# Kernel tuning notes

Hardware: AMD Instinct MI355X
Metric: run time of the kernel (lower is better)

Reference implementation:

```python
import jax, jax.numpy as jnp
import numpy as np

HIDDEN = 512
INPUT = 512
BATCH = 16384


def _quant_dequant(w):
    # mirrors torch: scale = max(|w|)/127 + 1e-8; int8 round-clamp; dequantize
    scale = jnp.max(jnp.abs(w)) / 127.0 + 1e-8
    q = jnp.clip(jnp.round(w / scale), -128, 127)
    return q * scale


def setup_inputs() -> dict:
    key = jax.random.key(0)
    ks = jax.random.split(key, 7)
    x = jax.random.normal(ks[0], (BATCH, INPUT), dtype=jnp.float32)
    h_prev = jax.random.normal(ks[1], (BATCH, HIDDEN), dtype=jnp.float32)
    c_prev = jax.random.normal(ks[2], (BATCH, HIDDEN), dtype=jnp.float32)
    w_ih = _quant_dequant(jax.random.normal(ks[3], (4 * HIDDEN, INPUT), dtype=jnp.float32) * 0.05)
    w_hh = _quant_dequant(jax.random.normal(ks[4], (4 * HIDDEN, HIDDEN), dtype=jnp.float32) * 0.05)
    bias_ih = jax.random.normal(ks[5], (4 * HIDDEN,), dtype=jnp.float32) * 0.05
    bias_hh = jax.random.normal(ks[6], (4 * HIDDEN,), dtype=jnp.float32) * 0.05
    return {"x": x, "h_prev": h_prev, "c_prev": c_prev,
            "w_ih": w_ih, "w_hh": w_hh, "bias_ih": bias_ih, "bias_hh": bias_hh}


def reference(x, h_prev, c_prev, w_ih, w_hh, bias_ih, bias_hh):
    # gates: [B, 4H]
    gates = x @ w_ih.T + bias_ih + h_prev @ w_hh.T + bias_hh
    i_g, f_g, g_g, o_g = jnp.split(gates, 4, axis=1)
    i_g = jax.nn.sigmoid(i_g)
    f_g = jax.nn.sigmoid(f_g)
    g_g = jnp.tanh(g_g)
    o_g = jax.nn.sigmoid(o_g)
    c_new = f_g * c_prev + i_g * g_g
    h_new = o_g * jnp.tanh(c_new)
    return (h_new, c_new)
```

## Files before the change

kernel.cpp:

```cpp
#include <hip/hip_runtime.h>


typedef __attribute__((ext_vector_type(4))) int int4v;
typedef __attribute__((ext_vector_type(8))) short short8;
typedef __attribute__((ext_vector_type(4))) float f32x4;
typedef unsigned int u32;
typedef unsigned short u16;
typedef unsigned char u8;

#define BATCH 16384
#define HID 512
#define KTOT 1024
#define BM 256
#define KSTEPS 16
#define TILEA_BYTES 16384
#define TILEW_BYTES 4096
#define NBM 64
#define NBN 32
#define WSA_BYTES ((size_t)NBM * KSTEPS * TILEA_BYTES)
#define WSW_BYTES ((size_t)NBN * KSTEPS * TILEW_BYTES)
#define SCALE_OFF (WSA_BYTES + WSW_BYTES)
#define PART_OFF (SCALE_OFF + 65536)
#define SW_OFF (PART_OFF + 2048)
#define WS_NEEDED (SW_OFF + 64)
#define PACKA_BLOCKS (BATCH / 4)

__device__ __forceinline__ float sigmoidf_(float v) { return 1.0f / (1.0f + __expf(-v)); }
__device__ __forceinline__ float tanhf_(float v) { return 1.0f - 2.0f / (__expf(2.0f * v) + 1.0f); }

__device__ __forceinline__ u32 pack4(float a, float b, float c, float d, float inv) {
    int q0 = (int)rintf(a * inv), q1 = (int)rintf(b * inv);
    int q2 = (int)rintf(c * inv), q3 = (int)rintf(d * inv);
    return (q0 & 255) | ((q1 & 255) << 8) | ((q2 & 255) << 16) | ((q3 & 255) << 24);
}

__global__ __launch_bounds__(256) void pack_a_wmax(
    const float* __restrict__ x, const float* __restrict__ h_prev,
    const float* __restrict__ w_ih, const float* __restrict__ w_hh,
    u8* __restrict__ wsA, float* __restrict__ aScale, float* __restrict__ part)
{
    const u32 t = threadIdx.x;
    if (blockIdx.x >= PACKA_BLOCKS) {
        const u32 b = blockIdx.x - PACKA_BLOCKS;
        const float* src = (b < 256) ? (w_ih + (size_t)b * 4096)
                                     : (w_hh + (size_t)(b - 256) * 4096);
        float am = 0.f;
        const float4* p = (const float4*)src + t;
        #pragma unroll
        for (int j = 0; j < 4; ++j) {
            float4 v = p[j * 256];
            am = fmaxf(am, fmaxf(fmaxf(fabsf(v.x), fabsf(v.y)), fmaxf(fabsf(v.z), fabsf(v.w))));
        }
        #pragma unroll
        for (int o = 32; o >= 1; o >>= 1) am = fmaxf(am, __shfl_xor(am, o, 64));
        __shared__ float red[4];
        if ((t & 63) == 0) red[t >> 6] = am;
        __syncthreads();
        if (t == 0) part[b] = fmaxf(fmaxf(red[0], red[1]), fmaxf(red[2], red[3]));
        return;
    }
    __shared__ float4 stg[4][256];
    const u32 lane = t & 63;
    const u32 wv = t >> 6;
    const u32 m = blockIdx.x * 4 + wv;
    const float4* xr = (const float4*)(x + (size_t)m * 512);
    const float4* hr = (const float4*)(h_prev + (size_t)m * 512);
    float4 v[4];
    v[0] = xr[lane];
    v[1] = xr[lane + 64];
    v[2] = hr[lane];
    v[3] = hr[lane + 64];
    float am = 0.f;
    #pragma unroll
    for (int j = 0; j < 4; ++j)
        am = fmaxf(am, fmaxf(fmaxf(fabsf(v[j].x), fabsf(v[j].y)),
                             fmaxf(fabsf(v[j].z), fabsf(v[j].w))));
    #pragma unroll
    for (int o = 32; o >= 1; o >>= 1) am = fmaxf(am, __shfl_xor(am, o, 64));
    const float inv = (am > 0.f) ? 127.0f / am : 0.f;
    if (lane == 0) aScale[m] = am * (1.0f / 127.0f);

    #pragma unroll
    for (int j = 0; j < 4; ++j)
        stg[wv][j * 64 + (lane ^ ((lane >> 2) & 7))] = v[j];
    u32 wds[4];
    #pragma unroll
    for (int s = 0; s < 4; ++s) {
        float4 w = stg[wv][(4 * lane + s) ^ (lane & 7)];
        wds[s] = pack4(w.x, w.y, w.z, w.w, inv);
    }
    const u32 bm = m >> 8, row = m & 255;
    const u32 ks = lane >> 2, kc = lane & 3;
    const u32 chunk = ((row >> 4) << 6) | (kc << 4) | (row & 15);
    int4v val = {(int)wds[0], (int)wds[1], (int)wds[2], (int)wds[3]};
    *(int4v*)(wsA + (((size_t)bm * KSTEPS + ks) * 1024 + chunk) * 16) = val;
}

__global__ __launch_bounds__(256) void pack_w(
    const float* __restrict__ w_ih, const float* __restrict__ w_hh,
    const float* __restrict__ part, u8* __restrict__ wsW, float* __restrict__ swOut)
{
    const u32 t = threadIdx.x;
    float am = fmaxf(part[t], part[t + 256]);
    #pragma unroll
    for (int o = 32; o >= 1; o >>= 1) am = fmaxf(am, __shfl_xor(am, o, 64));
    __shared__ float red[4];
    if ((t & 63) == 0) red[t >> 6] = am;
    __syncthreads();
    const float wmax = fmaxf(fmaxf(red[0], red[1]), fmaxf(red[2], red[3]));
    const float inv = 127.0f / wmax;
    if (blockIdx.x == 0 && t == 0) *swOut = wmax * (1.0f / 127.0f);

    const u32 widx = blockIdx.x * 256 + t;
    const u32 tile = widx >> 8;
    const u32 ks = tile & 15, bn = tile >> 4;
    const u32 g = (widx >> 6) & 3;
    const u32 lane = widx & 63;
    const u32 kc = lane >> 4, colin = lane & 15;
    const u32 wr = g * 512 + bn * 16 + colin;
    const u32 kglob = ks * 64 + kc * 16;
    const float* src = (kglob < 512) ? (w_ih + (size_t)wr * 512 + kglob)
                                     : (w_hh + (size_t)wr * 512 + (kglob - 512));
    u32 wds[4];
    #pragma unroll
    for (int j = 0; j < 4; ++j) {
        float4 v = *((const float4*)src + j);
        wds[j] = pack4(v.x, v.y, v.z, v.w, inv);
    }
    int4v val = {(int)wds[0], (int)wds[1], (int)wds[2], (int)wds[3]};
    *(int4v*)(wsW + (size_t)widx * 16) = val;
}

__global__ __launch_bounds__(256, 4) void lstm_gemm(
    const u8* __restrict__ wsA, const u8* __restrict__ wsW,
    const float* __restrict__ aScale, const float* __restrict__ swPtr,
    const float* __restrict__ c_prev,
    const float* __restrict__ b_ih, const float* __restrict__ b_hh,
    float* __restrict__ h_out, float* __restrict__ c_out)
{
    const int t = threadIdx.x;
    const u32 bid = blockIdx.x;
    const u32 xcd = bid & 7;
    const u32 slot = bid >> 3;
    const int bm = (int)((slot >> 5) * 8 + xcd);
    const int bn = (int)(slot & 31);
    const int n0 = bn * 16;
    const int rowBase = bm * BM;

    const int lane = t & 63;
    const int wv = t >> 6;
    const int colin = lane & 15;
    const int quad = lane >> 4;

    int4v acc[4][4];
    #pragma unroll
    for (int rf = 0; rf < 4; ++rf)
        #pragma unroll
        for (int g = 0; g < 4; ++g)
            acc[rf][g] = (int4v){0, 0, 0, 0};

    const char* gA = (const char*)wsA + (size_t)bm * KSTEPS * TILEA_BYTES
                     + (size_t)(wv * 4) * 1024 + (size_t)lane * 16;
    const char* gW = (const char*)wsW + (size_t)bn * KSTEPS * TILEW_BYTES
                     + (size_t)lane * 16;

#define LOADF(KS, AF, WF)                                                       \
    {                                                                           \
        _Pragma("unroll")                                                       \
        for (int rf = 0; rf < 4; ++rf)                                          \
            AF[rf] = *(const int4v*)(gA + (size_t)(KS) * TILEA_BYTES + rf * 1024); \
        _Pragma("unroll")                                                       \
        for (int g = 0; g < 4; ++g)                                             \
            WF[g] = *(const int4v*)(gW + (size_t)(KS) * TILEW_BYTES + g * 1024);   \
    }

#define COMPUTEF(AF, WF)                                                        \
    {                                                                           \
        _Pragma("unroll")                                                       \
        for (int rf = 0; rf < 4; ++rf)                                          \
            _Pragma("unroll")                                                   \
            for (int g = 0; g < 4; ++g)                                         \
                acc[rf][g] = __builtin_amdgcn_mfma_i32_16x16x64_i8(             \
                    AF[rf], WF[g], acc[rf][g], 0, 0, 0);                        \
    }

    int4v af0[4], wf0[4], af1[4], wf1[4];
    LOADF(0, af0, wf0);
    #pragma unroll 1
    for (int ks = 0; ks < KSTEPS; ks += 2) {
        LOADF(ks + 1, af1, wf1);
        COMPUTEF(af0, wf0);
        if (ks + 2 < KSTEPS) LOADF(ks + 2, af0, wf0);
        COMPUTEF(af1, wf1);
    }
#undef LOADF
#undef COMPUTEF

    const float sw = *swPtr;
    const int colg = n0 + colin;
    float bsum[4];
    #pragma unroll
    for (int g = 0; g < 4; ++g)
        bsum[g] = b_ih[g * 512 + colg] + b_hh[g * 512 + colg];

    #pragma unroll
    for (int rf = 0; rf < 4; ++rf) {
        #pragma unroll
        for (int reg = 0; reg < 4; ++reg) {
            const int row = rowBase + wv * 64 + rf * 16 + quad * 4 + reg;
            const size_t off = (size_t)row * 512 + colg;
            const float s = aScale[row] * sw;
            const float ig = (float)acc[rf][0][reg] * s + bsum[0];
            const float fg = (float)acc[rf][1][reg] * s + bsum[1];
            const float gg = (float)acc[rf][2][reg] * s + bsum[2];
            const float og = (float)acc[rf][3][reg] * s + bsum[3];
            const float cp = __builtin_nontemporal_load(c_prev + off);
            const float cn = sigmoidf_(fg) * cp + sigmoidf_(ig) * tanhf_(gg);
            const float hn = sigmoidf_(og) * tanhf_(cn);
            __builtin_nontemporal_store(hn, h_out + off);
            __builtin_nontemporal_store(cn, c_out + off);
        }
    }
}

#define LDSK 72
__device__ __forceinline__ u16 f2bf(float f) {
    u32 u = __builtin_bit_cast(u32, f);
    u += 0x7FFFu + ((u >> 16) & 1u);
    return (u16)(u >> 16);
}
__global__ __launch_bounds__(256, 3) void lstm_fused_v1(
    const float* __restrict__ x, const float* __restrict__ h_prev,
    const float* __restrict__ c_prev, const float* __restrict__ w_ih,
    const float* __restrict__ w_hh, const float* __restrict__ b_ih,
    const float* __restrict__ b_hh, float* __restrict__ h_out,
    float* __restrict__ c_out)
{
    __shared__ u16 sA[128][LDSK];
    __shared__ u16 sW[128][LDSK];
    const int t = threadIdx.x;
    const int bn = blockIdx.x & 15, bm = blockIdx.x >> 4;
    const int n0 = bn * 32, rowBase = bm * 128;
    const int srow = t >> 4, scol = t & 15;
    const int lane = t & 63, wv = t >> 6, colin = lane & 15, quad = lane >> 4;
    f32x4 acc[2][2][4];
    #pragma unroll
    for (int rf = 0; rf < 2; ++rf)
        #pragma unroll
        for (int cc = 0; cc < 2; ++cc)
            #pragma unroll
            for (int g = 0; g < 4; ++g) acc[rf][cc][g] = (f32x4){0.f, 0.f, 0.f, 0.f};
    for (int k0 = 0; k0 < KTOT; k0 += 64) {
        const int kk = (k0 < 512) ? k0 : (k0 - 512);
        const float* aSrc = (k0 < 512) ? x : h_prev;
        const float* wSrc = (k0 < 512) ? w_ih : w_hh;
        __syncthreads();
        #pragma unroll
        for (int p = 0; p < 8; ++p) {
            const int r = srow + p * 16;
            const float4 av = *(const float4*)(aSrc + (size_t)(rowBase + r) * 512 + kk + scol * 4);
            ushort4 ap; ap.x = f2bf(av.x); ap.y = f2bf(av.y); ap.z = f2bf(av.z); ap.w = f2bf(av.w);
            *(ushort4*)&sA[r][scol * 4] = ap;
            const int gate = r >> 5, rr = r & 31;
            const float4 wvv = *(const float4*)(wSrc + (size_t)(gate * 512 + n0 + rr) * 512 + kk + scol * 4);
            ushort4 wp; wp.x = f2bf(wvv.x); wp.y = f2bf(wvv.y); wp.z = f2bf(wvv.z); wp.w = f2bf(wvv.w);
            *(ushort4*)&sW[r][scol * 4] = wp;
        }
        __syncthreads();
        #pragma unroll
        for (int ks = 0; ks < 2; ++ks) {
            short8 af[2];
            #pragma unroll
            for (int rf = 0; rf < 2; ++rf)
                af[rf] = *(const short8*)&sA[wv * 32 + rf * 16 + colin][ks * 32 + quad * 8];
            short8 bfr[2][4];
            #pragma unroll
            for (int cc = 0; cc < 2; ++cc)
                #pragma unroll
                for (int g = 0; g < 4; ++g)
                    bfr[cc][g] = *(const short8*)&sW[g * 32 + cc * 16 + colin][ks * 32 + quad * 8];
            #pragma unroll
            for (int rf = 0; rf < 2; ++rf)
                #pragma unroll
                for (int cc = 0; cc < 2; ++cc)
                    #pragma unroll
                    for (int g = 0; g < 4; ++g)
                        acc[rf][cc][g] = __builtin_amdgcn_mfma_f32_16x16x32_bf16(
                            af[rf], bfr[cc][g], acc[rf][cc][g], 0, 0, 0);
        }
    }
    float bsum[2][4];
    #pragma unroll
    for (int cc = 0; cc < 2; ++cc) {
        const int colg = n0 + cc * 16 + colin;
        #pragma unroll
        for (int g = 0; g < 4; ++g) bsum[cc][g] = b_ih[g * 512 + colg] + b_hh[g * 512 + colg];
    }
    #pragma unroll
    for (int rf = 0; rf < 2; ++rf)
        #pragma unroll
        for (int cc = 0; cc < 2; ++cc) {
            const int colg = n0 + cc * 16 + colin;
            #pragma unroll
            for (int reg = 0; reg < 4; ++reg) {
                const int row = rowBase + wv * 32 + rf * 16 + quad * 4 + reg;
                const size_t off = (size_t)row * 512 + colg;
                const float ig = acc[rf][cc][0][reg] + bsum[cc][0];
                const float fg = acc[rf][cc][1][reg] + bsum[cc][1];
                const float gg = acc[rf][cc][2][reg] + bsum[cc][2];
                const float og = acc[rf][cc][3][reg] + bsum[cc][3];
                const float cp = c_prev[off];
                const float cn = sigmoidf_(fg) * cp + sigmoidf_(ig) * tanhf_(gg);
                const float hn = sigmoidf_(og) * tanhf_(cn);
                h_out[off] = hn;
                c_out[off] = cn;
            }
        }
}

extern "C" void kernel_launch(void* const* d_in, const int* in_sizes, int n_in,
                              void* d_out, int out_size, void* d_ws, size_t ws_size,
                              hipStream_t stream) {
    const float* x      = (const float*)d_in[0];
    const float* h_prev = (const float*)d_in[1];
    const float* c_prev = (const float*)d_in[2];
    const float* w_ih   = (const float*)d_in[3];
    const float* w_hh   = (const float*)d_in[4];
    const float* b_ih   = (const float*)d_in[5];
    const float* b_hh   = (const float*)d_in[6];
    float* h_out = (float*)d_out;
    float* c_out = h_out + (size_t)BATCH * HID;

    if (ws_size >= WS_NEEDED) {
        u8* wsA = (u8*)d_ws;
        u8* wsW = (u8*)d_ws + WSA_BYTES;
        float* aScale = (float*)((char*)d_ws + SCALE_OFF);
        float* part   = (float*)((char*)d_ws + PART_OFF);
        float* swOut  = (float*)((char*)d_ws + SW_OFF);
        pack_a_wmax<<<PACKA_BLOCKS + 512, 256, 0, stream>>>(x, h_prev, w_ih, w_hh,
                                                            wsA, aScale, part);
        pack_w<<<512, 256, 0, stream>>>(w_ih, w_hh, part, wsW, swOut);
        lstm_gemm<<<NBM * NBN, 256, 0, stream>>>(wsA, wsW, aScale, swOut, c_prev,
                                                 b_ih, b_hh, h_out, c_out);
    } else {
        lstm_fused_v1<<<128 * 16, 256, 0, stream>>>(x, h_prev, c_prev, w_ih, w_hh,
                                                    b_ih, b_hh, h_out, c_out);
    }
}
```

Baseline: 220.0 us.

## Restructure activation int8 packing to 16 rows per block with coalesced chunk writes

Result: slower. 224.9 us (+2.2%).

```diff
diff --git a/kernel.cpp b/kernel.cpp
--- a/kernel.cpp
+++ b/kernel.cpp
@@ -23,7 +23,7 @@
 #define PART_OFF (SCALE_OFF + 65536)
 #define SW_OFF (PART_OFF + 2048)
 #define WS_NEEDED (SW_OFF + 64)
-#define PACKA_BLOCKS (BATCH / 4)
+#define PACKA_BLOCKS 1024
 
 __device__ __forceinline__ float sigmoidf_(float v) { return 1.0f / (1.0f + __expf(-v)); }
 __device__ __forceinline__ float tanhf_(float v) { return 1.0f - 2.0f / (__expf(2.0f * v) + 1.0f); }
@@ -53,47 +53,63 @@
         }
         #pragma unroll
         for (int o = 32; o >= 1; o >>= 1) am = fmaxf(am, __shfl_xor(am, o, 64));
-        __shared__ float red[4];
-        if ((t & 63) == 0) red[t >> 6] = am;
+        __shared__ float redw[4];
+        if ((t & 63) == 0) redw[t >> 6] = am;
         __syncthreads();
-        if (t == 0) part[b] = fmaxf(fmaxf(red[0], red[1]), fmaxf(red[2], red[3]));
+        if (t == 0) part[b] = fmaxf(fmaxf(redw[0], redw[1]), fmaxf(redw[2], redw[3]));
         return;
     }
-    __shared__ float4 stg[4][256];
-    const u32 lane = t & 63;
-    const u32 wv = t >> 6;
-    const u32 m = blockIdx.x * 4 + wv;
-    const float4* xr = (const float4*)(x + (size_t)m * 512);
-    const float4* hr = (const float4*)(h_prev + (size_t)m * 512);
-    float4 v[4];
-    v[0] = xr[lane];
-    v[1] = xr[lane + 64];
-    v[2] = hr[lane];
-    v[3] = hr[lane + 64];
-    float am = 0.f;
-    #pragma unroll
-    for (int j = 0; j < 4; ++j)
-        am = fmaxf(am, fmaxf(fmaxf(fabsf(v[j].x), fabsf(v[j].y)),
-                             fmaxf(fabsf(v[j].z), fabsf(v[j].w))));
-    #pragma unroll
-    for (int o = 32; o >= 1; o >>= 1) am = fmaxf(am, __shfl_xor(am, o, 64));
+    const u32 S = blockIdx.x;
+    const u32 bm = S >> 4;
+    const u32 rowgrp = S & 15;
+    const size_t rowBase = (size_t)S * 16;
+
+    float m[16];
+    #pragma unroll
+    for (int j = 0; j < 16; ++j) {
+        const float4 v = (t < 128)
+            ? ((const float4*)(x + (rowBase + j) * 512))[t]
+            : ((const float4*)(h_prev + (rowBase + j) * 512))[t - 128];
+        m[j] = fmaxf(fmaxf(fabsf(v.x), fabsf(v.y)), fmaxf(fabsf(v.z), fabsf(v.w)));
+    }
+    #pragma unroll
+    for (int j = 0; j < 16; ++j)
+        #pragma unroll
+        for (int o = 32; o >= 1; o >>= 1)
+            m[j] = fmaxf(m[j], __shfl_xor(m[j], o, 64));
+
+    __shared__ float red[4][16];
+    const u32 wv = t >> 6, lane = t & 63;
+    if (lane == 0) {
+        #pragma unroll
+        for (int j = 0; j < 16; ++j) red[wv][j] = m[j];
+    }
+    __syncthreads();
+    const u32 rowin = t & 15;
+    const float am = fmaxf(fmaxf(red[0][rowin], red[1][rowin]),
+                           fmaxf(red[2][rowin], red[3][rowin]));
     const float inv = (am > 0.f) ? 127.0f / am : 0.f;
-    if (lane == 0) aScale[m] = am * (1.0f / 127.0f);
-
-    #pragma unroll
-    for (int j = 0; j < 4; ++j)
-        stg[wv][j * 64 + (lane ^ ((lane >> 2) & 7))] = v[j];
-    u32 wds[4];
-    #pragma unroll
-    for (int s = 0; s < 4; ++s) {
-        float4 w = stg[wv][(4 * lane + s) ^ (lane & 7)];
-        wds[s] = pack4(w.x, w.y, w.z, w.w, inv);
-    }
-    const u32 bm = m >> 8, row = m & 255;
-    const u32 ks = lane >> 2, kc = lane & 3;
-    const u32 chunk = ((row >> 4) << 6) | (kc << 4) | (row & 15);
-    int4v val = {(int)wds[0], (int)wds[1], (int)wds[2], (int)wds[3]};
-    *(int4v*)(wsA + (((size_t)bm * KSTEPS + ks) * 1024 + chunk) * 16) = val;
+    if (t < 16) aScale[rowBase + t] = am * (1.0f / 127.0f);
+
+    #pragma unroll
+    for (int it = 0; it < 4; ++it) {
+        const u32 chunkid = it * 256 + t;
+        const u32 ks = chunkid >> 6;
+        const u32 c = chunkid & 63;
+        const u32 kc = c >> 4;
+        const u32 f4b = ks * 16 + kc * 4;
+        const float4* srcb = (ks < 8)
+            ? (const float4*)(x + (rowBase + rowin) * 512) + f4b
+            : (const float4*)(h_prev + (rowBase + rowin) * 512) + (f4b - 128);
+        u32 wds[4];
+        #pragma unroll
+        for (int q = 0; q < 4; ++q) {
+            float4 v = srcb[q];
+            wds[q] = pack4(v.x, v.y, v.z, v.w, inv);
+        }
+        int4v val = {(int)wds[0], (int)wds[1], (int)wds[2], (int)wds[3]};
+        *(int4v*)(wsA + (((size_t)(bm * KSTEPS + ks)) * 1024 + rowgrp * 64 + c) * 16) = val;
+    }
 }
 
 __global__ __launch_bounds__(256) void pack_w(
```
